# Optimization experiments

Hardware: AMD Instinct MI355X
Metric: run time of the kernel (lower is better)

The kernel has to match this reference:

```python
import jax, jax.numpy as jnp
import numpy as np

B1, B2, D = 8192, 12288, 128


def setup_inputs() -> dict:
    key = jax.random.key(0)
    k1, k2 = jax.random.split(key)
    desc1 = jax.random.normal(k1, (B1, D), dtype=jnp.float32)
    desc2 = jax.random.normal(k2, (B2, D), dtype=jnp.float32)
    return {"desc1": desc1, "desc2": desc2}


def reference(desc1, desc2):
    # Pairwise L2 distance (torch.cdist, p=2) via the expanded form to avoid
    sq1 = jnp.sum(desc1 * desc1, axis=1, keepdims=True)          # (B1, 1)
    sq2 = jnp.sum(desc2 * desc2, axis=1)                          # (B2,)
    cost = jnp.sqrt(jnp.maximum(sq1 + sq2 - 2.0 * (desc1 @ desc2.T), 0.0))  # (B1, B2)

    b1, b2 = cost.shape
    ms = min(b1, b2)

    match_dists = jnp.min(cost, axis=1)    # (B1,) row minima
    idxs_in_2 = jnp.argmin(cost, axis=1)   # (B1,)
    match_dists2 = jnp.min(cost, axis=0)   # (B2,) col minima
    idxs_in_1 = jnp.argmin(cost, axis=0)   # (B2,)

    minsize_idxs = jnp.arange(ms)
    if b1 <= b2:  # static shape comparison -> Python if is fine
        mutual_nns = minsize_idxs == idxs_in_1[idxs_in_2][:ms]
        dists = match_dists[:ms]
        matches_idxs = jnp.stack([minsize_idxs, idxs_in_2[:ms]], axis=1)
    else:
        mutual_nns = minsize_idxs == idxs_in_2[idxs_in_1][:ms]
        dists = match_dists2[:ms]
        matches_idxs = jnp.stack([idxs_in_1[:ms], minsize_idxs], axis=1)

    # jit-compatible fixed-size output: non-mutual rows are masked with
    # dist=+inf and idx=-1 instead of boolean-compressed as in torch.
    match_dists_out = jnp.where(mutual_nns, dists, jnp.inf).reshape(-1, 1)  # (ms, 1)
    matches_idxs_out = jnp.where(mutual_nns[:, None], matches_idxs, -1)      # (ms, 2)
    return match_dists_out, matches_idxs_out, mutual_nns
```

## Files before the change

### kernel.cpp

```cpp
#include <hip/hip_runtime.h>
#include <math.h>

#define NB1 8192
#define NB2 12288
#define DD  128

typedef unsigned long long u64;
typedef unsigned short ushort_t;
typedef __attribute__((ext_vector_type(8))) short short8;
typedef __attribute__((ext_vector_type(4))) float f32x4;

__device__ __forceinline__ float bigf() { return __uint_as_float(0x7F7F0000u); }

__device__ __forceinline__ unsigned orderbits(float v) {
    unsigned b = __float_as_uint(v);
    return b ^ ((unsigned)((int)b >> 31) | 0x80000000u);
}
__device__ __forceinline__ float unorderbits(unsigned k) {
    unsigned b = (k & 0x80000000u) ? (k ^ 0x80000000u) : ~k;
    return __uint_as_float(b);
}
__device__ __forceinline__ u64 packkey(float v, unsigned idx) {
    return ((u64)orderbits(v) << 32) | idx;
}
__device__ __forceinline__ u64 umin64(u64 a, u64 b) { return a < b ? a : b; }

__device__ __forceinline__ ushort_t bf_rn(float x) {
    unsigned u = __float_as_uint(x);
    return (ushort_t)((u + 0x7FFFu + ((u >> 16) & 1u)) >> 16);
}
__device__ __forceinline__ float bf_up(ushort_t h) {
    return __uint_as_float(((unsigned)h) << 16);
}
__device__ __forceinline__ int fswz(int r) { return (r + (r >> 2)) & 3; }
__device__ __forceinline__ short8 ld8(const ushort_t* p) { return *(const short8*)p; }

__global__ __launch_bounds__(256) void prep_kernel(
    const float* __restrict__ d1, const float* __restrict__ d2,
    float* __restrict__ sq1, float* __restrict__ sq2,
    u64* __restrict__ rowmin, u64* __restrict__ colmin) {
    int t = blockIdx.x * 256 + threadIdx.x;
    if (t < NB1) {
        rowmin[t] = ~0ull;
        const float4* p = (const float4*)(d1 + (size_t)t * DD);
        float s = 0.f;
        #pragma unroll
        for (int c = 0; c < DD / 4; ++c) {
            float4 v = p[c];
            s = fmaf(v.x, v.x, s); s = fmaf(v.y, v.y, s);
            s = fmaf(v.z, v.z, s); s = fmaf(v.w, v.w, s);
        }
        sq1[t] = s;
    }
    if (t < NB2) {
        colmin[t] = ~0ull;
        const float4* p = (const float4*)(d2 + (size_t)t * DD);
        float s = 0.f;
        #pragma unroll
        for (int c = 0; c < DD / 4; ++c) {
            float4 v = p[c];
            s = fmaf(v.x, v.x, s); s = fmaf(v.y, v.y, s);
            s = fmaf(v.z, v.z, s); s = fmaf(v.w, v.w, s);
        }
        sq2[t] = s;
    }
}

__global__ __launch_bounds__(256) void split_frag_kernel(
    const float* __restrict__ d1, const float* __restrict__ d2,
    ushort_t* __restrict__ Af, ushort_t* __restrict__ Bf) {
    int t = blockIdx.x * 256 + threadIdx.x;
    int lane = t & 63;
    int task = t >> 6;
    bool isA = task < 2048;
    int lt = isA ? task : task - 2048;
    int rb = lt >> 2;
    int kc = lt & 3;
    int row = rb * 16 + (lane & 15);
    int kst = kc * 32 + (lane >> 4) * 8;
    const float* src = (isA ? d1 : d2) + (size_t)row * DD + kst;
    ushort_t* dst = (isA ? Af : Bf) + ((size_t)lt * 1536 + lane * 8);

    short8 H, M, L;
    #pragma unroll
    for (int e = 0; e < 8; ++e) {
        float x = src[e];
        ushort_t h = bf_rn(x); float r1 = x - bf_up(h);
        ushort_t m = bf_rn(r1); float r2 = r1 - bf_up(m);
        H[e] = (short)h; M[e] = (short)m; L[e] = (short)bf_rn(r2);
    }
    *(short8*)(dst)        = H;
    *(short8*)(dst + 512)  = M;
    *(short8*)(dst + 1024) = L;
}

__global__ __launch_bounds__(256) void mfma_tile3_kernel(
    const ushort_t* __restrict__ Af, const ushort_t* __restrict__ Bf,
    const float* __restrict__ sq1, const float* __restrict__ sq2,
    u64* __restrict__ rowmin, u64* __restrict__ colmin)
{
    const int bid  = blockIdx.x;
    const int xcd  = bid & 7;
    const int t_   = bid >> 3;
    const int kch  = t_ >> 6;
    const int wdn  = t_ & 63;
    const int cj   = wdn & 7;
    const int ci   = wdn >> 3;
    const int j0b  = (kch * 8 + cj) * 128;
    const int i0b  = (xcd * 8 + ci) * 128;

    const int tid  = threadIdx.x;
    const int lane = tid & 63;
    const int wid  = tid >> 6;
    const int wr   = wid >> 1;
    const int wc   = wid & 1;
    const int lrow = lane & 15;
    const int lg   = lane >> 4;

    const ushort_t* abase = Af + ((size_t)((i0b >> 4) + wr * 4) * 6144) + lane * 8;
    const ushort_t* bbase = Bf + ((size_t)((j0b >> 4) + wc * 4) * 6144) + lane * 8;

    f32x4 acc[4][4];
    #pragma unroll
    for (int mi = 0; mi < 4; ++mi)
        #pragma unroll
        for (int ni = 0; ni < 4; ++ni)
            acc[mi][ni] = (f32x4){0.f, 0.f, 0.f, 0.f};

    short8 bufA[3][4], bufB[3][4];
    short8 a0[3], a1[3];
    #pragma unroll
    for (int c = 0; c < 3; ++c) {
        #pragma unroll
        for (int ni = 0; ni < 4; ++ni)
            bufA[c][ni] = ld8(bbase + ni * 6144 + c * 512);
        a0[c] = ld8(abase + c * 512);
    }

    #pragma unroll
    for (int kc = 0; kc < 4; ++kc) {
        short8 (&bc)[3][4] = (kc & 1) ? bufB : bufA;
        short8 (&bn)[3][4] = (kc & 1) ? bufA : bufB;
        if (kc < 3) {
            #pragma unroll
            for (int c = 0; c < 3; ++c)
                #pragma unroll
                for (int ni = 0; ni < 4; ++ni)
                    bn[c][ni] = ld8(bbase + ni * 6144 + (kc + 1) * 1536 + c * 512);
        }
        #pragma unroll
        for (int mi = 0; mi < 4; ++mi) {
            if (mi < 3) {
                #pragma unroll
                for (int c = 0; c < 3; ++c)
                    a1[c] = ld8(abase + (mi + 1) * 6144 + kc * 1536 + c * 512);
            } else if (kc < 3) {
                #pragma unroll
                for (int c = 0; c < 3; ++c)
                    a1[c] = ld8(abase + (kc + 1) * 1536 + c * 512);
            }
            #pragma unroll
            for (int ni = 0; ni < 4; ++ni) {
                f32x4 a = acc[mi][ni];
                a = __builtin_amdgcn_mfma_f32_16x16x32_bf16(a0[0], bc[0][ni], a, 0, 0, 0);
                a = __builtin_amdgcn_mfma_f32_16x16x32_bf16(a0[0], bc[1][ni], a, 0, 0, 0);
                a = __builtin_amdgcn_mfma_f32_16x16x32_bf16(a0[1], bc[0][ni], a, 0, 0, 0);
                a = __builtin_amdgcn_mfma_f32_16x16x32_bf16(a0[0], bc[2][ni], a, 0, 0, 0);
                a = __builtin_amdgcn_mfma_f32_16x16x32_bf16(a0[1], bc[1][ni], a, 0, 0, 0);
                a = __builtin_amdgcn_mfma_f32_16x16x32_bf16(a0[2], bc[0][ni], a, 0, 0, 0);
                acc[mi][ni] = a;
            }
            #pragma unroll
            for (int c = 0; c < 3; ++c) a0[c] = a1[c];
        }
    }

    float q2v[4];
    #pragma unroll
    for (int ni = 0; ni < 4; ++ni)
        q2v[ni] = sq2[j0b + wc * 64 + ni * 16 + lrow];
    float4 q1v[4];
    #pragma unroll
    for (int mi = 0; mi < 4; ++mi)
        q1v[mi] = *(const float4*)(sq1 + i0b + wr * 64 + mi * 16 + 4 * lg);

    #pragma unroll
    for (int mi = 0; mi < 4; ++mi)
        #pragma unroll
        for (int r = 0; r < 4; ++r) {
            u64 best = ~0ull;
            #pragma unroll
            for (int ni = 0; ni < 4; ++ni) {
                float kr = fmaf(-2.f, acc[mi][ni][r], q2v[ni]);
                best = umin64(best, packkey(kr, (unsigned)(j0b + wc * 64 + ni * 16 + lrow)));
            }
            #pragma unroll
            for (int mask = 8; mask; mask >>= 1)
                best = umin64(best, __shfl_xor(best, mask));
            if (lrow == 0)
                atomicMin(&rowmin[i0b + wr * 64 + mi * 16 + 4 * lg + r], best);
        }

    #pragma unroll
    for (int ni = 0; ni < 4; ++ni) {
        u64 best = ~0ull;
        #pragma unroll
        for (int mi = 0; mi < 4; ++mi) {
            const float* q1p = (const float*)&q1v[mi];
            #pragma unroll
            for (int r = 0; r < 4; ++r) {
                float kc_ = fmaf(-2.f, acc[mi][ni][r], q1p[r]);
                best = umin64(best, packkey(kc_, (unsigned)(i0b + wr * 64 + mi * 16 + 4 * lg + r)));
            }
        }
        best = umin64(best, __shfl_xor(best, 16));
        best = umin64(best, __shfl_xor(best, 32));
        if (lane < 16)
            atomicMin(&colmin[j0b + wc * 64 + ni * 16 + lrow], best);
    }
}

__global__ __launch_bounds__(256) void mfma_tile_kernel(
    const float* __restrict__ d1, const float* __restrict__ d2,
    const float* __restrict__ sq1, const float* __restrict__ sq2,
    u64* __restrict__ rowmin, u64* __restrict__ colmin)
{
    __shared__ __align__(16) short lds[6 * 4096];
    const int tid = threadIdx.x;
    const int i0b = blockIdx.y * 128;
    const int j0b = blockIdx.x * 128;
    const int srow  = tid >> 1;
    const int shalf = tid & 1;
    const int sfr   = fswz(srow);
    const int sg0   = ((2 * shalf) ^ sfr) * 8;
    const int sg1   = ((2 * shalf + 1) ^ sfr) * 8;
    const float* gA = d1 + (size_t)(i0b + srow) * DD + shalf * 16;
    const float* gB = d2 + (size_t)(j0b + srow) * DD + shalf * 16;
    short* wA = lds + srow * 32;
    short* wB = lds + 3 * 4096 + srow * 32;
    const int lane = tid & 63;
    const int wid  = tid >> 6;
    const int wr   = wid >> 1;
    const int wc   = wid & 1;
    const int lrow = lane & 15;
    const int lg   = lane >> 4;
    const int gx   = (lg ^ fswz(lrow)) * 8;
    const int aoff = (wr * 64 + lrow) * 32 + gx;
    const int boff = 3 * 4096 + (wc * 64 + lrow) * 32 + gx;

    f32x4 acc[4][4];
    #pragma unroll
    for (int mi = 0; mi < 4; ++mi)
        #pragma unroll
        for (int ni = 0; ni < 4; ++ni)
            acc[mi][ni] = (f32x4){0.f, 0.f, 0.f, 0.f};

    for (int kc = 0; kc < 4; ++kc) {
        {
            const float* sp = gA + kc * 32;
            short8 H0, M0, L0, H1, M1, L1;
            #pragma unroll
            for (int e = 0; e < 8; ++e) {
                float x = sp[e];
                ushort_t h = bf_rn(x); float r1 = x - bf_up(h);
                ushort_t m = bf_rn(r1); float r2 = r1 - bf_up(m);
                H0[e] = (short)h; M0[e] = (short)m; L0[e] = (short)bf_rn(r2);
            }
            #pragma unroll
            for (int e = 0; e < 8; ++e) {
                float x = sp[8 + e];
                ushort_t h = bf_rn(x); float r1 = x - bf_up(h);
                ushort_t m = bf_rn(r1); float r2 = r1 - bf_up(m);
                H1[e] = (short)h; M1[e] = (short)m; L1[e] = (short)bf_rn(r2);
            }
            *(short8*)(wA + sg0)        = H0;
            *(short8*)(wA + sg1)        = H1;
            *(short8*)(wA + 4096 + sg0) = M0;
            *(short8*)(wA + 4096 + sg1) = M1;
            *(short8*)(wA + 8192 + sg0) = L0;
            *(short8*)(wA + 8192 + sg1) = L1;
        }
        {
            const float* sp = gB + kc * 32;
            short8 H0, M0, L0, H1, M1, L1;
            #pragma unroll
            for (int e = 0; e < 8; ++e) {
                float x = sp[e];
                ushort_t h = bf_rn(x); float r1 = x - bf_up(h);
                ushort_t m = bf_rn(r1); float r2 = r1 - bf_up(m);
                H0[e] = (short)h; M0[e] = (short)m; L0[e] = (short)bf_rn(r2);
            }
            #pragma unroll
            for (int e = 0; e < 8; ++e) {
                float x = sp[8 + e];
                ushort_t h = bf_rn(x); float r1 = x - bf_up(h);
                ushort_t m = bf_rn(r1); float r2 = r1 - bf_up(m);
                H1[e] = (short)h; M1[e] = (short)m; L1[e] = (short)bf_rn(r2);
            }
            *(short8*)(wB + sg0)        = H0;
            *(short8*)(wB + sg1)        = H1;
            *(short8*)(wB + 4096 + sg0) = M0;
            *(short8*)(wB + 4096 + sg1) = M1;
            *(short8*)(wB + 8192 + sg0) = L0;
            *(short8*)(wB + 8192 + sg1) = L1;
        }
        __syncthreads();
        short8 af[3][4], bfr[3][4];
        #pragma unroll
        for (int c = 0; c < 3; ++c)
            #pragma unroll
            for (int t = 0; t < 4; ++t) {
                af[c][t]  = *(const short8*)(lds + c * 4096 + aoff + t * 512);
                bfr[c][t] = *(const short8*)(lds + c * 4096 + boff + t * 512);
            }
        #pragma unroll
        for (int mi = 0; mi < 4; ++mi)
            #pragma unroll
            for (int ni = 0; ni < 4; ++ni) {
                f32x4 a = acc[mi][ni];
                a = __builtin_amdgcn_mfma_f32_16x16x32_bf16(af[0][mi], bfr[0][ni], a, 0, 0, 0);
                a = __builtin_amdgcn_mfma_f32_16x16x32_bf16(af[0][mi], bfr[1][ni], a, 0, 0, 0);
                a = __builtin_amdgcn_mfma_f32_16x16x32_bf16(af[1][mi], bfr[0][ni], a, 0, 0, 0);
                a = __builtin_amdgcn_mfma_f32_16x16x32_bf16(af[0][mi], bfr[2][ni], a, 0, 0, 0);
                a = __builtin_amdgcn_mfma_f32_16x16x32_bf16(af[1][mi], bfr[1][ni], a, 0, 0, 0);
                a = __builtin_amdgcn_mfma_f32_16x16x32_bf16(af[2][mi], bfr[0][ni], a, 0, 0, 0);
                acc[mi][ni] = a;
            }
        __syncthreads();
    }

    float q2v[4];
    #pragma unroll
    for (int ni = 0; ni < 4; ++ni)
        q2v[ni] = sq2[j0b + wc * 64 + ni * 16 + lrow];
    float4 q1v[4];
    #pragma unroll
    for (int mi = 0; mi < 4; ++mi)
        q1v[mi] = *(const float4*)(sq1 + i0b + wr * 64 + mi * 16 + 4 * lg);

    #pragma unroll
    for (int mi = 0; mi < 4; ++mi)
        #pragma unroll
        for (int r = 0; r < 4; ++r) {
            u64 best = ~0ull;
            #pragma unroll
            for (int ni = 0; ni < 4; ++ni) {
                float kr = fmaf(-2.f, acc[mi][ni][r], q2v[ni]);
                best = umin64(best, packkey(kr, (unsigned)(j0b + wc * 64 + ni * 16 + lrow)));
            }
            #pragma unroll
            for (int mask = 8; mask; mask >>= 1)
                best = umin64(best, __shfl_xor(best, mask));
            if (lrow == 0)
                atomicMin(&rowmin[i0b + wr * 64 + mi * 16 + 4 * lg + r], best);
        }
    #pragma unroll
    for (int ni = 0; ni < 4; ++ni) {
        u64 best = ~0ull;
        #pragma unroll
        for (int mi = 0; mi < 4; ++mi) {
            const float* q1p = (const float*)&q1v[mi];
            #pragma unroll
            for (int r = 0; r < 4; ++r) {
                float kc_ = fmaf(-2.f, acc[mi][ni][r], q1p[r]);
                best = umin64(best, packkey(kc_, (unsigned)(i0b + wr * 64 + mi * 16 + 4 * lg + r)));
            }
        }
        best = umin64(best, __shfl_xor(best, 16));
        best = umin64(best, __shfl_xor(best, 32));
        if (lane < 16)
            atomicMin(&colmin[j0b + wc * 64 + ni * 16 + lrow], best);
    }
}

__global__ __launch_bounds__(256) void final_kernel(
    const float* __restrict__ sq1,
    const u64* __restrict__ rowmin, const u64* __restrict__ colmin,
    float* __restrict__ out) {
    int i = blockIdx.x * 256 + threadIdx.x;
    if (i >= NB1) return;
    u64 rm = rowmin[i];
    unsigned ju = (unsigned)(rm & 0xFFFFFFFFu);
    float kr = unorderbits((unsigned)(rm >> 32));
    float dist = sqrtf(fmaxf(sq1[i] + kr, 0.f));
    dist = fminf(dist, bigf());
    bool valid = (ju < (unsigned)NB2);
    int j = valid ? (int)ju : 0;
    u64 cm = colmin[j];
    int i2 = (int)(cm & 0xFFFFFFFFu);
    bool mut = valid && (i2 == i);
    out[i] = mut ? dist : bigf();
    out[NB1 + 2 * i]     = mut ? (float)i : -1.f;
    out[NB1 + 2 * i + 1] = mut ? (float)j : -1.f;
    out[NB1 + 2 * NB1 + i] = mut ? 1.f : 0.f;
}

extern "C" void kernel_launch(void* const* d_in, const int* in_sizes, int n_in,
                              void* d_out, int out_size, void* d_ws, size_t ws_size,
                              hipStream_t stream) {
    const float* d1 = (const float*)d_in[0];
    const float* d2 = (const float*)d_in[1];
    float* out = (float*)d_out;

    char* ws = (char*)d_ws;
    float* sq1    = (float*)(ws);
    float* sq2    = (float*)(ws + 32768);
    u64*   rowmin = (u64*)(ws + 81920);
    u64*   colmin = (u64*)(ws + 147456);
    ushort_t* Af = (ushort_t*)(ws + 245760);
    ushort_t* Bf = (ushort_t*)(ws + 245760 + 6291456);
    const size_t need = 245760 + 6291456 + 9437184;

    hipLaunchKernelGGL(prep_kernel, dim3((NB2 + 255) / 256), dim3(256), 0, stream,
                       d1, d2, sq1, sq2, rowmin, colmin);
    if (ws_size >= need) {
        hipLaunchKernelGGL(split_frag_kernel, dim3(1280), dim3(256), 0, stream,
                           d1, d2, Af, Bf);
        hipLaunchKernelGGL(mfma_tile3_kernel, dim3((NB2 / 128) * (NB1 / 128)), dim3(256), 0, stream,
                           Af, Bf, sq1, sq2, rowmin, colmin);
    } else {
        hipLaunchKernelGGL(mfma_tile_kernel, dim3(NB2 / 128, NB1 / 128), dim3(256), 0, stream,
                           d1, d2, sq1, sq2, rowmin, colmin);
    }
    hipLaunchKernelGGL(final_kernel, dim3((NB1 + 255) / 256), dim3(256), 0, stream,
                       sq1, rowmin, colmin, out);
}
```

Measured before the change: 195.2 us.

## Use concatenated-K bf16x3 GEMM with LDS double-buffered 256x128 tiles

Adds a split kernel that writes the hi/mid/lo bf16 parts of each row into a 768-wide K layout. The pairing is arranged so that a plain GEMM over K=768 reproduces the six cross-product MFMAs. A new GEMM kernel uses 256x128 block tiles, loads global memory directly into swizzled LDS with double buffering, and uses setprio and barriers to schedule the MFMAs, so each fragment is reused from LDS instead of streamed per wave from global. The split buffers double in size and need a larger workspace. The fallback path without the fused-split kernel is removed, so a small workspace now skips the GEMM.

```diff
diff --git a/kernel.cpp b/kernel.cpp
--- a/kernel.cpp
+++ b/kernel.cpp
@@ -4,6 +4,8 @@
 #define NB1 8192
 #define NB2 12288
 #define DD  128
+#define KE  768
+#define NKT 24
 
 typedef unsigned long long u64;
 typedef unsigned short ushort_t;
@@ -32,8 +34,12 @@
 __device__ __forceinline__ float bf_up(ushort_t h) {
     return __uint_as_float(((unsigned)h) << 16);
 }
-__device__ __forceinline__ int fswz(int r) { return (r + (r >> 2)) & 3; }
-__device__ __forceinline__ short8 ld8(const ushort_t* p) { return *(const short8*)p; }
+
+__device__ __forceinline__ void gload_lds16(const void* g, void* l) {
+    __builtin_amdgcn_global_load_lds(
+        (const __attribute__((address_space(1))) unsigned*)g,
+        (__attribute__((address_space(3))) unsigned*)l, 16, 0, 0);
+}
 
 __global__ __launch_bounds__(256) void prep_kernel(
     const float* __restrict__ d1, const float* __restrict__ d2,
@@ -63,6 +69,193 @@
             s = fmaf(v.z, v.z, s); s = fmaf(v.w, v.w, s);
         }
         sq2[t] = s;
+    }
+}
+
+__global__ __launch_bounds__(256) void split_gemm_kernel(
+    const float* __restrict__ d1, const float* __restrict__ d2,
+    ushort_t* __restrict__ Ap, ushort_t* __restrict__ Bp) {
+    int t = blockIdx.x * 256 + threadIdx.x;
+    int row = t >> 2, q = t & 3;
+    bool isA = row < NB1;
+    int r = isA ? row : row - NB1;
+    const float* src = (isA ? d1 + (size_t)r * DD : d2 + (size_t)r * DD) + q * 32;
+    ushort_t* dst = (isA ? Ap : Bp) + (size_t)r * KE + q * 32;
+
+    #pragma unroll
+    for (int v = 0; v < 4; ++v) {
+        short8 H, M, L;
+        #pragma unroll
+        for (int e = 0; e < 8; ++e) {
+            float x = src[v * 8 + e];
+            ushort_t h = bf_rn(x); float r1 = x - bf_up(h);
+            ushort_t m = bf_rn(r1); float r2 = r1 - bf_up(m);
+            H[e] = (short)h; M[e] = (short)m; L[e] = (short)bf_rn(r2);
+        }
+        if (isA) {
+            *(short8*)(dst + 0   + v * 8) = H;
+            *(short8*)(dst + 128 + v * 8) = H;
+            *(short8*)(dst + 384 + v * 8) = H;
+            *(short8*)(dst + 256 + v * 8) = M;
+            *(short8*)(dst + 512 + v * 8) = M;
+            *(short8*)(dst + 640 + v * 8) = L;
+        } else {
+            *(short8*)(dst + 0   + v * 8) = H;
+            *(short8*)(dst + 256 + v * 8) = H;
+            *(short8*)(dst + 640 + v * 8) = H;
+            *(short8*)(dst + 128 + v * 8) = M;
+            *(short8*)(dst + 512 + v * 8) = M;
+            *(short8*)(dst + 384 + v * 8) = L;
+        }
+    }
+}
+
+__global__ __launch_bounds__(256, 2) void mfma_tile4_kernel(
+    const ushort_t* __restrict__ Ap, const ushort_t* __restrict__ Bp,
+    const float* __restrict__ sq1, const float* __restrict__ sq2,
+    u64* __restrict__ rowmin, u64* __restrict__ colmin)
+{
+    __shared__ __align__(16) short sA[2][8192];
+    __shared__ __align__(16) short sB[2][4096];
+
+    const int bid = blockIdx.x;
+    const int xcd = bid & 7;
+    const int t_  = bid >> 3;
+    const int ch  = t_ >> 5;
+    const int w_  = t_ & 31;
+    const int i0b = (xcd * 4 + (w_ >> 3)) * 256;
+    const int j0b = (ch * 8 + (w_ & 7)) * 128;
+
+    const int tid  = threadIdx.x;
+    const int lane = tid & 63;
+    const int wid  = tid >> 6;
+    const int wr   = wid >> 1;
+    const int wc   = wid & 1;
+    const int lrow = lane & 15;
+    const int lg   = lane >> 4;
+
+    const int sr4 = tid >> 2;
+    const int ss  = tid & 3;
+
+    const ushort_t* Asrc = Ap + (size_t)i0b * KE;
+    const ushort_t* Bsrc = Bp + (size_t)j0b * KE;
+
+    f32x4 acc[8][4];
+    #pragma unroll
+    for (int m = 0; m < 8; ++m)
+        #pragma unroll
+        for (int n = 0; n < 4; ++n)
+            acc[m][n] = (f32x4){0.f, 0.f, 0.f, 0.f};
+
+    #define STAGE_A(Ts, cb) do {                                              \
+        _Pragma("unroll")                                                     \
+        for (int i_ = 0; i_ < 4; ++i_) {                                      \
+            int r_ = i_ * 64 + sr4;                                           \
+            int g_ = ss ^ ((r_ >> 1) & 3);                                    \
+            gload_lds16(Asrc + (size_t)r_ * KE + (Ts) * 32 + g_ * 8,          \
+                        &sA[cb][r_ * 32 + ss * 8]);                           \
+        } } while (0)
+    #define STAGE_B(Ts, cb) do {                                              \
+        _Pragma("unroll")                                                     \
+        for (int i_ = 0; i_ < 2; ++i_) {                                      \
+            int r_ = i_ * 64 + sr4;                                           \
+            int g_ = ss ^ ((r_ >> 1) & 3);                                    \
+            gload_lds16(Bsrc + (size_t)r_ * KE + (Ts) * 32 + g_ * 8,          \
+                        &sB[cb][r_ * 32 + ss * 8]);                           \
+        } } while (0)
+
+    STAGE_A(0, 0); STAGE_B(0, 0);
+    asm volatile("s_waitcnt vmcnt(0)" ::: "memory");
+    __builtin_amdgcn_s_barrier();
+
+    short8 aF[4], bF[4];
+    for (int T = 0; T < NKT; ++T) {
+        const int c = T & 1;
+        #pragma unroll
+        for (int n = 0; n < 4; ++n) {
+            int r = wc * 64 + n * 16 + lrow;
+            bF[n] = *(const short8*)&sB[c][r * 32 + (lg ^ ((r >> 1) & 3)) * 8];
+        }
+        #pragma unroll
+        for (int m = 0; m < 4; ++m) {
+            int r = wr * 128 + m * 16 + lrow;
+            aF[m] = *(const short8*)&sA[c][r * 32 + (lg ^ ((r >> 1) & 3)) * 8];
+        }
+        if (T + 1 < NKT) { STAGE_A(T + 1, c ^ 1); STAGE_B(T + 1, c ^ 1); }
+        __builtin_amdgcn_s_barrier();
+        asm volatile("s_waitcnt lgkmcnt(0)" ::: "memory");
+        __builtin_amdgcn_sched_barrier(0);
+        __builtin_amdgcn_s_setprio(1);
+        #pragma unroll
+        for (int m = 0; m < 4; ++m)
+            #pragma unroll
+            for (int n = 0; n < 4; ++n)
+                acc[m][n] = __builtin_amdgcn_mfma_f32_16x16x32_bf16(aF[m], bF[n], acc[m][n], 0, 0, 0);
+        __builtin_amdgcn_s_setprio(0);
+        __builtin_amdgcn_s_barrier();
+        #pragma unroll
+        for (int m = 0; m < 4; ++m) {
+            int r = wr * 128 + (m + 4) * 16 + lrow;
+            aF[m] = *(const short8*)&sA[c][r * 32 + (lg ^ ((r >> 1) & 3)) * 8];
+        }
+        __builtin_amdgcn_s_barrier();
+        asm volatile("s_waitcnt lgkmcnt(0)" ::: "memory");
+        __builtin_amdgcn_sched_barrier(0);
+        __builtin_amdgcn_s_setprio(1);
+        #pragma unroll
+        for (int m = 0; m < 4; ++m)
+            #pragma unroll
+            for (int n = 0; n < 4; ++n)
+                acc[m + 4][n] = __builtin_amdgcn_mfma_f32_16x16x32_bf16(aF[m], bF[n], acc[m + 4][n], 0, 0, 0);
+        __builtin_amdgcn_s_setprio(0);
+        asm volatile("s_waitcnt vmcnt(0)" ::: "memory");
+        __builtin_amdgcn_s_barrier();
+    }
+    #undef STAGE_A
+    #undef STAGE_B
+
+    float q2v[4];
+    #pragma unroll
+    for (int n = 0; n < 4; ++n)
+        q2v[n] = sq2[j0b + wc * 64 + n * 16 + lrow];
+    float4 q1v[8];
+    #pragma unroll
+    for (int m = 0; m < 8; ++m)
+        q1v[m] = *(const float4*)(sq1 + i0b + wr * 128 + m * 16 + 4 * lg);
+
+    #pragma unroll
+    for (int m = 0; m < 8; ++m)
+        #pragma unroll
+        for (int r = 0; r < 4; ++r) {
+            u64 best = ~0ull;
+            #pragma unroll
+            for (int n = 0; n < 4; ++n) {
+                float kr = fmaf(-2.f, acc[m][n][r], q2v[n]);
+                best = umin64(best, packkey(kr, (unsigned)(j0b + wc * 64 + n * 16 + lrow)));
+            }
+            #pragma unroll
+            for (int mask = 8; mask; mask >>= 1)
+                best = umin64(best, __shfl_xor(best, mask));
+            if (lrow == 0)
+                atomicMin(&rowmin[i0b + wr * 128 + m * 16 + 4 * lg + r], best);
+        }
+
+    #pragma unroll
+    for (int n = 0; n < 4; ++n) {
+        u64 best = ~0ull;
+        #pragma unroll
+        for (int m = 0; m < 8; ++m) {
+            const float* q1p = (const float*)&q1v[m];
+            #pragma unroll
+            for (int r = 0; r < 4; ++r) {
+                float kc_ = fmaf(-2.f, acc[m][n][r], q1p[r]);
+                best = umin64(best, packkey(kc_, (unsigned)(i0b + wr * 128 + m * 16 + 4 * lg + r)));
+            }
+        }
+        best = umin64(best, __shfl_xor(best, 16));
+        best = umin64(best, __shfl_xor(best, 32));
+        if (lane < 16)
+            atomicMin(&colmin[j0b + wc * 64 + n * 16 + lrow], best);
     }
 }
 
@@ -80,7 +273,6 @@
     int kst = kc * 32 + (lane >> 4) * 8;
     const float* src = (isA ? d1 : d2) + (size_t)row * DD + kst;
     ushort_t* dst = (isA ? Af : Bf) + ((size_t)lt * 1536 + lane * 8);
-
     short8 H, M, L;
     #pragma unroll
     for (int e = 0; e < 8; ++e) {
@@ -93,6 +285,8 @@
     *(short8*)(dst + 512)  = M;
     *(short8*)(dst + 1024) = L;
 }
+
+__device__ __forceinline__ short8 ld8f(const ushort_t* p) { return *(const short8*)p; }
 
 __global__ __launch_bounds__(256) void mfma_tile3_kernel(
     const ushort_t* __restrict__ Af, const ushort_t* __restrict__ Bf,
@@ -104,11 +298,8 @@
     const int t_   = bid >> 3;
     const int kch  = t_ >> 6;
     const int wdn  = t_ & 63;
-    const int cj   = wdn & 7;
-    const int ci   = wdn >> 3;
-    const int j0b  = (kch * 8 + cj) * 128;
-    const int i0b  = (xcd * 8 + ci) * 128;
-
+    const int j0b  = (kch * 8 + (wdn & 7)) * 128;
+    const int i0b  = (xcd * 8 + (wdn >> 3)) * 128;
     const int tid  = threadIdx.x;
     const int lane = tid & 63;
     const int wid  = tid >> 6;
@@ -116,7 +307,6 @@
     const int wc   = wid & 1;
     const int lrow = lane & 15;
     const int lg   = lane >> 4;
-
     const ushort_t* abase = Af + ((size_t)((i0b >> 4) + wr * 4) * 6144) + lane * 8;
     const ushort_t* bbase = Bf + ((size_t)((j0b >> 4) + wc * 4) * 6144) + lane * 8;
 
@@ -133,10 +323,9 @@
     for (int c = 0; c < 3; ++c) {
         #pragma unroll
         for (int ni = 0; ni < 4; ++ni)
-            bufA[c][ni] = ld8(bbase + ni * 6144 + c * 512);
-        a0[c] = ld8(abase + c * 512);
-    }
-
+            bufA[c][ni] = ld8f(bbase + ni * 6144 + c * 512);
+        a0[c] = ld8f(abase + c * 512);
+    }
     #pragma unroll
     for (int kc = 0; kc < 4; ++kc) {
         short8 (&bc)[3][4] = (kc & 1) ? bufB : bufA;
@@ -146,18 +335,18 @@
             for (int c = 0; c < 3; ++c)
                 #pragma unroll
                 for (int ni = 0; ni < 4; ++ni)
-                    bn[c][ni] = ld8(bbase + ni * 6144 + (kc + 1) * 1536 + c * 512);
+                    bn[c][ni] = ld8f(bbase + ni * 6144 + (kc + 1) * 1536 + c * 512);
         }
         #pragma unroll
         for (int mi = 0; mi < 4; ++mi) {
             if (mi < 3) {
                 #pragma unroll
                 for (int c = 0; c < 3; ++c)
-                    a1[c] = ld8(abase + (mi + 1) * 6144 + kc * 1536 + c * 512);
+                    a1[c] = ld8f(abase + (mi + 1) * 6144 + kc * 1536 + c * 512);
             } else if (kc < 3) {
                 #pragma unroll
                 for (int c = 0; c < 3; ++c)
-                    a1[c] = ld8(abase + (kc + 1) * 1536 + c * 512);
+                    a1[c] = ld8f(abase + (kc + 1) * 1536 + c * 512);
             }
             #pragma unroll
             for (int ni = 0; ni < 4; ++ni) {
@@ -174,7 +363,6 @@
             for (int c = 0; c < 3; ++c) a0[c] = a1[c];
         }
     }
-
     float q2v[4];
     #pragma unroll
     for (int ni = 0; ni < 4; ++ni)
@@ -183,161 +371,6 @@
     #pragma unroll
     for (int mi = 0; mi < 4; ++mi)
         q1v[mi] = *(const float4*)(sq1 + i0b + wr * 64 + mi * 16 + 4 * lg);
-
-    #pragma unroll
-    for (int mi = 0; mi < 4; ++mi)
-        #pragma unroll
-        for (int r = 0; r < 4; ++r) {
-            u64 best = ~0ull;
-            #pragma unroll
-            for (int ni = 0; ni < 4; ++ni) {
-                float kr = fmaf(-2.f, acc[mi][ni][r], q2v[ni]);
-                best = umin64(best, packkey(kr, (unsigned)(j0b + wc * 64 + ni * 16 + lrow)));
-            }
-            #pragma unroll
-            for (int mask = 8; mask; mask >>= 1)
-                best = umin64(best, __shfl_xor(best, mask));
-            if (lrow == 0)
-                atomicMin(&rowmin[i0b + wr * 64 + mi * 16 + 4 * lg + r], best);
-        }
-
-    #pragma unroll
-    for (int ni = 0; ni < 4; ++ni) {
-        u64 best = ~0ull;
-        #pragma unroll
-        for (int mi = 0; mi < 4; ++mi) {
-            const float* q1p = (const float*)&q1v[mi];
-            #pragma unroll
-            for (int r = 0; r < 4; ++r) {
-                float kc_ = fmaf(-2.f, acc[mi][ni][r], q1p[r]);
-                best = umin64(best, packkey(kc_, (unsigned)(i0b + wr * 64 + mi * 16 + 4 * lg + r)));
-            }
-        }
-        best = umin64(best, __shfl_xor(best, 16));
-        best = umin64(best, __shfl_xor(best, 32));
-        if (lane < 16)
-            atomicMin(&colmin[j0b + wc * 64 + ni * 16 + lrow], best);
-    }
-}
-
-__global__ __launch_bounds__(256) void mfma_tile_kernel(
-    const float* __restrict__ d1, const float* __restrict__ d2,
-    const float* __restrict__ sq1, const float* __restrict__ sq2,
-    u64* __restrict__ rowmin, u64* __restrict__ colmin)
-{
-    __shared__ __align__(16) short lds[6 * 4096];
-    const int tid = threadIdx.x;
-    const int i0b = blockIdx.y * 128;
-    const int j0b = blockIdx.x * 128;
-    const int srow  = tid >> 1;
-    const int shalf = tid & 1;
-    const int sfr   = fswz(srow);
-    const int sg0   = ((2 * shalf) ^ sfr) * 8;
-    const int sg1   = ((2 * shalf + 1) ^ sfr) * 8;
-    const float* gA = d1 + (size_t)(i0b + srow) * DD + shalf * 16;
-    const float* gB = d2 + (size_t)(j0b + srow) * DD + shalf * 16;
-    short* wA = lds + srow * 32;
-    short* wB = lds + 3 * 4096 + srow * 32;
-    const int lane = tid & 63;
-    const int wid  = tid >> 6;
-    const int wr   = wid >> 1;
-    const int wc   = wid & 1;
-    const int lrow = lane & 15;
-    const int lg   = lane >> 4;
-    const int gx   = (lg ^ fswz(lrow)) * 8;
-    const int aoff = (wr * 64 + lrow) * 32 + gx;
-    const int boff = 3 * 4096 + (wc * 64 + lrow) * 32 + gx;
-
-    f32x4 acc[4][4];
-    #pragma unroll
-    for (int mi = 0; mi < 4; ++mi)
-        #pragma unroll
-        for (int ni = 0; ni < 4; ++ni)
-            acc[mi][ni] = (f32x4){0.f, 0.f, 0.f, 0.f};
-
-    for (int kc = 0; kc < 4; ++kc) {
-        {
-            const float* sp = gA + kc * 32;
-            short8 H0, M0, L0, H1, M1, L1;
-            #pragma unroll
-            for (int e = 0; e < 8; ++e) {
-                float x = sp[e];
-                ushort_t h = bf_rn(x); float r1 = x - bf_up(h);
-                ushort_t m = bf_rn(r1); float r2 = r1 - bf_up(m);
-                H0[e] = (short)h; M0[e] = (short)m; L0[e] = (short)bf_rn(r2);
-            }
-            #pragma unroll
-            for (int e = 0; e < 8; ++e) {
-                float x = sp[8 + e];
-                ushort_t h = bf_rn(x); float r1 = x - bf_up(h);
-                ushort_t m = bf_rn(r1); float r2 = r1 - bf_up(m);
-                H1[e] = (short)h; M1[e] = (short)m; L1[e] = (short)bf_rn(r2);
-            }
-            *(short8*)(wA + sg0)        = H0;
-            *(short8*)(wA + sg1)        = H1;
-            *(short8*)(wA + 4096 + sg0) = M0;
-            *(short8*)(wA + 4096 + sg1) = M1;
-            *(short8*)(wA + 8192 + sg0) = L0;
-            *(short8*)(wA + 8192 + sg1) = L1;
-        }
-        {
-            const float* sp = gB + kc * 32;
-            short8 H0, M0, L0, H1, M1, L1;
-            #pragma unroll
-            for (int e = 0; e < 8; ++e) {
-                float x = sp[e];
-                ushort_t h = bf_rn(x); float r1 = x - bf_up(h);
-                ushort_t m = bf_rn(r1); float r2 = r1 - bf_up(m);
-                H0[e] = (short)h; M0[e] = (short)m; L0[e] = (short)bf_rn(r2);
-            }
-            #pragma unroll
-            for (int e = 0; e < 8; ++e) {
-                float x = sp[8 + e];
-                ushort_t h = bf_rn(x); float r1 = x - bf_up(h);
-                ushort_t m = bf_rn(r1); float r2 = r1 - bf_up(m);
-                H1[e] = (short)h; M1[e] = (short)m; L1[e] = (short)bf_rn(r2);
-            }
-            *(short8*)(wB + sg0)        = H0;
-            *(short8*)(wB + sg1)        = H1;
-            *(short8*)(wB + 4096 + sg0) = M0;
-            *(short8*)(wB + 4096 + sg1) = M1;
-            *(short8*)(wB + 8192 + sg0) = L0;
-            *(short8*)(wB + 8192 + sg1) = L1;
-        }
-        __syncthreads();
-        short8 af[3][4], bfr[3][4];
-        #pragma unroll
-        for (int c = 0; c < 3; ++c)
-            #pragma unroll
-            for (int t = 0; t < 4; ++t) {
-                af[c][t]  = *(const short8*)(lds + c * 4096 + aoff + t * 512);
-                bfr[c][t] = *(const short8*)(lds + c * 4096 + boff + t * 512);
-            }
-        #pragma unroll
-        for (int mi = 0; mi < 4; ++mi)
-            #pragma unroll
-            for (int ni = 0; ni < 4; ++ni) {
-                f32x4 a = acc[mi][ni];
-                a = __builtin_amdgcn_mfma_f32_16x16x32_bf16(af[0][mi], bfr[0][ni], a, 0, 0, 0);
-                a = __builtin_amdgcn_mfma_f32_16x16x32_bf16(af[0][mi], bfr[1][ni], a, 0, 0, 0);
-                a = __builtin_amdgcn_mfma_f32_16x16x32_bf16(af[1][mi], bfr[0][ni], a, 0, 0, 0);
-                a = __builtin_amdgcn_mfma_f32_16x16x32_bf16(af[0][mi], bfr[2][ni], a, 0, 0, 0);
-                a = __builtin_amdgcn_mfma_f32_16x16x32_bf16(af[1][mi], bfr[1][ni], a, 0, 0, 0);
-                a = __builtin_amdgcn_mfma_f32_16x16x32_bf16(af[2][mi], bfr[0][ni], a, 0, 0, 0);
-                acc[mi][ni] = a;
-            }
-        __syncthreads();
-    }
-
-    float q2v[4];
-    #pragma unroll
-    for (int ni = 0; ni < 4; ++ni)
-        q2v[ni] = sq2[j0b + wc * 64 + ni * 16 + lrow];
-    float4 q1v[4];
-    #pragma unroll
-    for (int mi = 0; mi < 4; ++mi)
-        q1v[mi] = *(const float4*)(sq1 + i0b + wr * 64 + mi * 16 + 4 * lg);
-
     #pragma unroll
     for (int mi = 0; mi < 4; ++mi)
         #pragma unroll
@@ -407,20 +440,25 @@
     float* sq2    = (float*)(ws + 32768);
     u64*   rowmin = (u64*)(ws + 81920);
     u64*   colmin = (u64*)(ws + 147456);
+    ushort_t* Ap = (ushort_t*)(ws + 245760);
+    ushort_t* Bp = (ushort_t*)(ws + 245760 + 12582912);
+    const size_t need2 = 245760 + 12582912 + 18874368;
     ushort_t* Af = (ushort_t*)(ws + 245760);
     ushort_t* Bf = (ushort_t*)(ws + 245760 + 6291456);
-    const size_t need = 245760 + 6291456 + 9437184;
+    const size_t need1 = 245760 + 6291456 + 9437184;
 
     hipLaunchKernelGGL(prep_kernel, dim3((NB2 + 255) / 256), dim3(256), 0, stream,
                        d1, d2, sq1, sq2, rowmin, colmin);
-    if (ws_size >= need) {
+    if (ws_size >= need2) {
+        hipLaunchKernelGGL(split_gemm_kernel, dim3(320), dim3(256), 0, stream,
+                           d1, d2, Ap, Bp);
+        hipLaunchKernelGGL(mfma_tile4_kernel, dim3(3072), dim3(256), 0, stream,
+                           Ap, Bp, sq1, sq2, rowmin, colmin);
+    } else if (ws_size >= need1) {
         hipLaunchKernelGGL(split_frag_kernel, dim3(1280), dim3(256), 0, stream,
                            d1, d2, Af, Bf);
-        hipLaunchKernelGGL(mfma_tile3_kernel, dim3((NB2 / 128) * (NB1 / 128)), dim3(256), 0, stream,
+        hipLaunchKernelGGL(mfma_tile3_kernel, dim3(6144), dim3(256), 0, stream,
                            Af, Bf, sq1, sq2, rowmin, colmin);
-    } else {
-        hipLaunchKernelGGL(mfma_tile_kernel, dim3(NB2 / 128, NB1 / 128), dim3(256), 0, stream,
-                           d1, d2, sq1, sq2, rowmin, colmin);
     }
     hipLaunchKernelGGL(final_kernel, dim3((NB1 + 255) / 256), dim3(256), 0, stream,
                        sq1, rowmin, colmin, out);
```

Result: slower. 244.6 us (+25.3%).

## Switch bf16x3 matmul to 32x32x16 MFMA with matching fragment layout

Applied to the files above, without the earlier changes.

Reorganizes the pre-split bf16 hi/mid/lo fragments into 32-row by 16-k blocks and replaces the 16x16x32 MFMA tile with 32x32x16 MFMA, each wave computing a 2x2 grid of 32x32 accumulators. The K loop now runs 8 chunks with double-buffered A and B fragment loads, and the row and column min epilogues are rewritten for the 32x32 output lane mapping. The aim is fewer MFMA issues and fewer operand loads per flop, since the larger instruction reuses each operand over more outputs. The cost is a different register footprint, and the row reduction needs a 5-step shuffle where the old one took 4.

```diff
diff --git a/kernel.cpp b/kernel.cpp
--- a/kernel.cpp
+++ b/kernel.cpp
@@ -9,6 +9,7 @@
 typedef unsigned short ushort_t;
 typedef __attribute__((ext_vector_type(8))) short short8;
 typedef __attribute__((ext_vector_type(4))) float f32x4;
+typedef __attribute__((ext_vector_type(16))) float f32x16;
 
 __device__ __forceinline__ float bigf() { return __uint_as_float(0x7F7F0000u); }
 
@@ -66,7 +67,7 @@
     }
 }
 
-__global__ __launch_bounds__(256) void split_frag_kernel(
+__global__ __launch_bounds__(256) void split_frag32_kernel(
     const float* __restrict__ d1, const float* __restrict__ d2,
     ushort_t* __restrict__ Af, ushort_t* __restrict__ Bf) {
     int t = blockIdx.x * 256 + threadIdx.x;
@@ -74,10 +75,10 @@
     int task = t >> 6;
     bool isA = task < 2048;
     int lt = isA ? task : task - 2048;
-    int rb = lt >> 2;
-    int kc = lt & 3;
-    int row = rb * 16 + (lane & 15);
-    int kst = kc * 32 + (lane >> 4) * 8;
+    int rb = lt >> 3;
+    int kc = lt & 7;
+    int row = rb * 32 + (lane & 31);
+    int kst = kc * 16 + (lane >> 5) * 8;
     const float* src = (isA ? d1 : d2) + (size_t)row * DD + kst;
     ushort_t* dst = (isA ? Af : Bf) + ((size_t)lt * 1536 + lane * 8);
 
@@ -94,7 +95,7 @@
     *(short8*)(dst + 1024) = L;
 }
 
-__global__ __launch_bounds__(256) void mfma_tile3_kernel(
+__global__ __launch_bounds__(256) void mfma_tile5_kernel(
     const ushort_t* __restrict__ Af, const ushort_t* __restrict__ Bf,
     const float* __restrict__ sq1, const float* __restrict__ sq2,
     u64* __restrict__ rowmin, u64* __restrict__ colmin)
@@ -104,119 +105,104 @@
     const int t_   = bid >> 3;
     const int kch  = t_ >> 6;
     const int wdn  = t_ & 63;
-    const int cj   = wdn & 7;
-    const int ci   = wdn >> 3;
-    const int j0b  = (kch * 8 + cj) * 128;
-    const int i0b  = (xcd * 8 + ci) * 128;
+    const int j0b  = (kch * 8 + (wdn & 7)) * 128;
+    const int i0b  = (xcd * 8 + (wdn >> 3)) * 128;
 
     const int tid  = threadIdx.x;
     const int lane = tid & 63;
     const int wid  = tid >> 6;
     const int wr   = wid >> 1;
     const int wc   = wid & 1;
-    const int lrow = lane & 15;
-    const int lg   = lane >> 4;
-
-    const ushort_t* abase = Af + ((size_t)((i0b >> 4) + wr * 4) * 6144) + lane * 8;
-    const ushort_t* bbase = Bf + ((size_t)((j0b >> 4) + wc * 4) * 6144) + lane * 8;
-
-    f32x4 acc[4][4];
-    #pragma unroll
-    for (int mi = 0; mi < 4; ++mi)
-        #pragma unroll
-        for (int ni = 0; ni < 4; ++ni)
-            acc[mi][ni] = (f32x4){0.f, 0.f, 0.f, 0.f};
-
-    short8 bufA[3][4], bufB[3][4];
-    short8 a0[3], a1[3];
-    #pragma unroll
-    for (int c = 0; c < 3; ++c) {
-        #pragma unroll
-        for (int ni = 0; ni < 4; ++ni)
-            bufA[c][ni] = ld8(bbase + ni * 6144 + c * 512);
-        a0[c] = ld8(abase + c * 512);
-    }
-
-    #pragma unroll
-    for (int kc = 0; kc < 4; ++kc) {
-        short8 (&bc)[3][4] = (kc & 1) ? bufB : bufA;
-        short8 (&bn)[3][4] = (kc & 1) ? bufA : bufB;
-        if (kc < 3) {
+    const int hi   = lane >> 5;
+    const int lc   = lane & 31;
+
+    const ushort_t* abase = Af + (size_t)((i0b >> 5) + wr * 2) * 12288 + lane * 8;
+    const ushort_t* bbase = Bf + (size_t)((j0b >> 5) + wc * 2) * 12288 + lane * 8;
+
+    f32x16 acc[2][2];
+    #pragma unroll
+    for (int mi = 0; mi < 2; ++mi)
+        #pragma unroll
+        for (int ni = 0; ni < 2; ++ni)
+            acc[mi][ni] = (f32x16)(0.f);
+
+    short8 ab[2][3][2], bb[2][3][2];
+    #pragma unroll
+    for (int c = 0; c < 3; ++c)
+        #pragma unroll
+        for (int x = 0; x < 2; ++x) {
+            ab[0][c][x] = ld8(abase + x * 12288 + c * 512);
+            bb[0][c][x] = ld8(bbase + x * 12288 + c * 512);
+        }
+
+    const int pa[6] = {0, 0, 1, 0, 1, 2};
+    const int pb[6] = {0, 1, 0, 2, 1, 0};
+
+    #pragma unroll
+    for (int kc = 0; kc < 8; ++kc) {
+        const int cb = kc & 1;
+        if (kc < 7) {
             #pragma unroll
             for (int c = 0; c < 3; ++c)
                 #pragma unroll
-                for (int ni = 0; ni < 4; ++ni)
-                    bn[c][ni] = ld8(bbase + ni * 6144 + (kc + 1) * 1536 + c * 512);
-        }
-        #pragma unroll
-        for (int mi = 0; mi < 4; ++mi) {
-            if (mi < 3) {
+                for (int x = 0; x < 2; ++x) {
+                    ab[cb ^ 1][c][x] = ld8(abase + x * 12288 + (kc + 1) * 1536 + c * 512);
+                    bb[cb ^ 1][c][x] = ld8(bbase + x * 12288 + (kc + 1) * 1536 + c * 512);
+                }
+        }
+        #pragma unroll
+        for (int p = 0; p < 6; ++p)
+            #pragma unroll
+            for (int mi = 0; mi < 2; ++mi)
                 #pragma unroll
-                for (int c = 0; c < 3; ++c)
-                    a1[c] = ld8(abase + (mi + 1) * 6144 + kc * 1536 + c * 512);
-            } else if (kc < 3) {
-                #pragma unroll
-                for (int c = 0; c < 3; ++c)
-                    a1[c] = ld8(abase + (kc + 1) * 1536 + c * 512);
-            }
-            #pragma unroll
-            for (int ni = 0; ni < 4; ++ni) {
-                f32x4 a = acc[mi][ni];
-                a = __builtin_amdgcn_mfma_f32_16x16x32_bf16(a0[0], bc[0][ni], a, 0, 0, 0);
-                a = __builtin_amdgcn_mfma_f32_16x16x32_bf16(a0[0], bc[1][ni], a, 0, 0, 0);
-                a = __builtin_amdgcn_mfma_f32_16x16x32_bf16(a0[1], bc[0][ni], a, 0, 0, 0);
-                a = __builtin_amdgcn_mfma_f32_16x16x32_bf16(a0[0], bc[2][ni], a, 0, 0, 0);
-                a = __builtin_amdgcn_mfma_f32_16x16x32_bf16(a0[1], bc[1][ni], a, 0, 0, 0);
-                a = __builtin_amdgcn_mfma_f32_16x16x32_bf16(a0[2], bc[0][ni], a, 0, 0, 0);
-                acc[mi][ni] = a;
-            }
-            #pragma unroll
-            for (int c = 0; c < 3; ++c) a0[c] = a1[c];
-        }
-    }
-
-    float q2v[4];
-    #pragma unroll
-    for (int ni = 0; ni < 4; ++ni)
-        q2v[ni] = sq2[j0b + wc * 64 + ni * 16 + lrow];
-    float4 q1v[4];
-    #pragma unroll
-    for (int mi = 0; mi < 4; ++mi)
-        q1v[mi] = *(const float4*)(sq1 + i0b + wr * 64 + mi * 16 + 4 * lg);
-
-    #pragma unroll
-    for (int mi = 0; mi < 4; ++mi)
-        #pragma unroll
-        for (int r = 0; r < 4; ++r) {
+                for (int ni = 0; ni < 2; ++ni)
+                    acc[mi][ni] = __builtin_amdgcn_mfma_f32_32x32x16_bf16(
+                        ab[cb][pa[p]][mi], bb[cb][pb[p]][ni], acc[mi][ni], 0, 0, 0);
+    }
+
+    float q2v[2];
+    #pragma unroll
+    for (int ni = 0; ni < 2; ++ni)
+        q2v[ni] = sq2[j0b + wc * 64 + ni * 32 + lc];
+    float4 q1v[2][4];
+    #pragma unroll
+    for (int mi = 0; mi < 2; ++mi)
+        #pragma unroll
+        for (int g = 0; g < 4; ++g)
+            q1v[mi][g] = *(const float4*)(sq1 + i0b + wr * 64 + mi * 32 + g * 8 + 4 * hi);
+
+    #pragma unroll
+    for (int mi = 0; mi < 2; ++mi)
+        #pragma unroll
+        for (int r = 0; r < 16; ++r) {
             u64 best = ~0ull;
             #pragma unroll
-            for (int ni = 0; ni < 4; ++ni) {
+            for (int ni = 0; ni < 2; ++ni) {
                 float kr = fmaf(-2.f, acc[mi][ni][r], q2v[ni]);
-                best = umin64(best, packkey(kr, (unsigned)(j0b + wc * 64 + ni * 16 + lrow)));
-            }
-            #pragma unroll
-            for (int mask = 8; mask; mask >>= 1)
+                best = umin64(best, packkey(kr, (unsigned)(j0b + wc * 64 + ni * 32 + lc)));
+            }
+            #pragma unroll
+            for (int mask = 16; mask; mask >>= 1)
                 best = umin64(best, __shfl_xor(best, mask));
-            if (lrow == 0)
-                atomicMin(&rowmin[i0b + wr * 64 + mi * 16 + 4 * lg + r], best);
-        }
-
-    #pragma unroll
-    for (int ni = 0; ni < 4; ++ni) {
+            if (lc == 0)
+                atomicMin(&rowmin[i0b + wr * 64 + mi * 32 + (r & 3) + 8 * (r >> 2) + 4 * hi], best);
+        }
+
+    #pragma unroll
+    for (int ni = 0; ni < 2; ++ni) {
         u64 best = ~0ull;
         #pragma unroll
-        for (int mi = 0; mi < 4; ++mi) {
-            const float* q1p = (const float*)&q1v[mi];
-            #pragma unroll
-            for (int r = 0; r < 4; ++r) {
-                float kc_ = fmaf(-2.f, acc[mi][ni][r], q1p[r]);
-                best = umin64(best, packkey(kc_, (unsigned)(i0b + wr * 64 + mi * 16 + 4 * lg + r)));
-            }
-        }
-        best = umin64(best, __shfl_xor(best, 16));
+        for (int mi = 0; mi < 2; ++mi)
+            #pragma unroll
+            for (int r = 0; r < 16; ++r) {
+                float q1 = ((const float*)&q1v[mi][r >> 2])[r & 3];
+                float kc_ = fmaf(-2.f, acc[mi][ni][r], q1);
+                best = umin64(best, packkey(kc_,
+                    (unsigned)(i0b + wr * 64 + mi * 32 + (r & 3) + 8 * (r >> 2) + 4 * hi)));
+            }
         best = umin64(best, __shfl_xor(best, 32));
-        if (lane < 16)
-            atomicMin(&colmin[j0b + wc * 64 + ni * 16 + lrow], best);
+        if (lane < 32)
+            atomicMin(&colmin[j0b + wc * 64 + ni * 32 + lc], best);
     }
 }
 
@@ -414,9 +400,9 @@
     hipLaunchKernelGGL(prep_kernel, dim3((NB2 + 255) / 256), dim3(256), 0, stream,
                        d1, d2, sq1, sq2, rowmin, colmin);
     if (ws_size >= need) {
-        hipLaunchKernelGGL(split_frag_kernel, dim3(1280), dim3(256), 0, stream,
+        hipLaunchKernelGGL(split_frag32_kernel, dim3(1280), dim3(256), 0, stream,
                            d1, d2, Af, Bf);
-        hipLaunchKernelGGL(mfma_tile3_kernel, dim3((NB2 / 128) * (NB1 / 128)), dim3(256), 0, stream,
+        hipLaunchKernelGGL(mfma_tile5_kernel, dim3(6144), dim3(256), 0, stream,
                            Af, Bf, sq1, sq2, rowmin, colmin);
     } else {
         hipLaunchKernelGGL(mfma_tile_kernel, dim3(NB2 / 128, NB1 / 128), dim3(256), 0, stream,
```

Result: slower. 252.7 us (+29.4%).
